# Kernel tuning notes

Measured on AMD Instinct MI355X. Metric: run time of the kernel, lower is better.

## Reference

```python
import jax, jax.numpy as jnp
import numpy as np

H, C = 2, 16          # heads, per-head channels (hidden_dim//2)
HD = H * C            # 32 = hidden_dim (concat heads)
NEG_SLOPE = 0.2       # PyG GATConv default negative_slope


def _gat(x, src, dst, edge_attr, lin_w, att_src, att_dst, edge_w, att_edge, bias):
    # Faithful PyG GATConv(in, C, heads=H, edge_dim=2, concat=True) in eval mode
    # (dropout inactive). add_self_loops=True with fill_value='mean' for edge_attr.
    N = x.shape[0]
    ones = jnp.ones((src.shape[0],), x.dtype)
    cnt = jax.ops.segment_sum(ones, dst, num_segments=N)
    mean_attr = jax.ops.segment_sum(edge_attr, dst, num_segments=N) / jnp.maximum(cnt, 1.0)[:, None]
    loop = jnp.arange(N, dtype=src.dtype)
    src_a = jnp.concatenate([src, loop])
    dst_a = jnp.concatenate([dst, loop])
    ea = jnp.concatenate([edge_attr, mean_attr], axis=0)            # [E+N, 2]
    xp = (x @ lin_w).reshape(N, H, C)                               # [N,H,C]
    a_src = (xp * att_src).sum(-1)                                  # [N,H]
    a_dst = (xp * att_dst).sum(-1)                                  # [N,H]
    ee = (ea @ edge_w).reshape(-1, H, C)                            # [E+N,H,C]
    a_edge = (ee * att_edge).sum(-1)                                # [E+N,H]
    alpha = jax.nn.leaky_relu(a_src[src_a] + a_dst[dst_a] + a_edge, NEG_SLOPE)
    m = jax.ops.segment_max(alpha, dst_a, num_segments=N)           # segment softmax over dst
    alpha = jnp.exp(alpha - m[dst_a])
    denom = jax.ops.segment_sum(alpha, dst_a, num_segments=N)
    alpha = alpha / (denom[dst_a] + 1e-16)
    msg = xp[src_a] * alpha[:, :, None]                             # [E+N,H,C]
    out = jax.ops.segment_sum(msg, dst_a, num_segments=N).reshape(N, HD)
    return out + bias


def _forward(group_ids, ord_feats, edge_index, edge_attr, pool_rows, pool_cols,
             pool_vals, P, embedding, g1, g2, g3, head_w1, head_b1, head_w2, head_b2):
    src, dst = edge_index[0], edge_index[1]
    x = jnp.concatenate([embedding[group_ids], ord_feats], axis=1)  # [N,20]
    h = jax.nn.relu(_gat(x, src, dst, edge_attr, *g1))
    h = jax.nn.relu(_gat(h, src, dst, edge_attr, *g2))
    h = jax.nn.relu(_gat(h, src, dst, edge_attr, *g3))              # [N,32]
    # sparse (P,N) Gaussian pooling matmul, COO form
    pooled = jax.ops.segment_sum(pool_vals[:, None] * h[pool_cols], pool_rows, num_segments=P)
    hh = jax.nn.relu(pooled @ head_w1 + head_b1)
    return (hh @ head_w2 + head_b2)[:, 0]                           # [P]


def setup_inputs() -> dict:
    key = jax.random.key(0)
    ks = jax.random.split(key, 32)
    N, E, P, NNZ, G = 100000, 3200000, 200000, 3200000, 19
    def nrm(k, shape, s=0.1):
        return jax.random.normal(k, shape, dtype=jnp.float32) * s
    inp = dict(
        group_ids=jax.random.randint(ks[0], (N,), 0, G, dtype=jnp.int32),
        ord_feats=jax.random.uniform(ks[1], (N, 4), dtype=jnp.float32),
        edge_index=jax.random.randint(ks[2], (2, E), 0, N, dtype=jnp.int32),
        edge_attr=jax.random.uniform(ks[3], (E, 2), dtype=jnp.float32),
        pool_rows=jax.random.randint(ks[4], (NNZ,), 0, P, dtype=jnp.int32),
        pool_cols=jax.random.randint(ks[5], (NNZ,), 0, N, dtype=jnp.int32),
        pool_vals=jax.random.uniform(ks[6], (NNZ,), dtype=jnp.float32),
        P=P,
        embedding=nrm(ks[7], (G, 16)),
    )
    ind = [20, HD, HD]
    for li in range(3):
        b = 8 + li * 6
        inp[f"g{li+1}_lin_w"] = nrm(ks[b], (ind[li], HD), (2.0 / (ind[li] + HD)) ** 0.5)
        inp[f"g{li+1}_att_src"] = nrm(ks[b + 1], (H, C))
        inp[f"g{li+1}_att_dst"] = nrm(ks[b + 2], (H, C))
        inp[f"g{li+1}_edge_w"] = nrm(ks[b + 3], (2, HD), 0.5)
        inp[f"g{li+1}_att_edge"] = nrm(ks[b + 4], (H, C))
        inp[f"g{li+1}_bias"] = jnp.zeros((HD,), jnp.float32)
    inp["head_w1"] = nrm(ks[26], (HD, 32), (2.0 / 64) ** 0.5)
    inp["head_b1"] = jnp.zeros((32,), jnp.float32)
    inp["head_w2"] = nrm(ks[27], (32, 1), (2.0 / 33) ** 0.5)
    inp["head_b2"] = jnp.zeros((1,), jnp.float32)
    return inp


def reference(group_ids, ord_feats, edge_index, edge_attr, pool_rows, pool_cols, pool_vals, P,
              embedding,
              g1_lin_w, g1_att_src, g1_att_dst, g1_edge_w, g1_att_edge, g1_bias,
              g2_lin_w, g2_att_src, g2_att_dst, g2_edge_w, g2_att_edge, g2_bias,
              g3_lin_w, g3_att_src, g3_att_dst, g3_edge_w, g3_att_edge, g3_bias,
              head_w1, head_b1, head_w2, head_b2):
    g1 = (g1_lin_w, g1_att_src, g1_att_dst, g1_edge_w, g1_att_edge, g1_bias)
    g2 = (g2_lin_w, g2_att_src, g2_att_dst, g2_edge_w, g2_att_edge, g2_bias)
    g3 = (g3_lin_w, g3_att_src, g3_att_dst, g3_edge_w, g3_att_edge, g3_bias)
    return _forward(group_ids, ord_feats, edge_index, edge_attr, pool_rows, pool_cols,
                    pool_vals, P, embedding, g1, g2, g3, head_w1, head_b1, head_w2, head_b2)
```

## Files before the change

### kernel.cpp

```cpp
#include <hip/hip_runtime.h>
#include <hip/hip_fp16.h>

#define TPB 256
#define STPB 1024
#define TILE 8192

__device__ __forceinline__ float leaky02(float x){ return x > 0.f ? x : 0.2f*x; }
__device__ __forceinline__ unsigned pack_h2(float a, float b){
  return (unsigned)__half_as_ushort(__float2half_rn(a)) |
         ((unsigned)__half_as_ushort(__float2half_rn(b)) << 16);
}

__global__ void k_scan_tile(const int* __restrict__ in, int* __restrict__ out,
                            int* __restrict__ bsum, int n) {
  __shared__ int sh[TPB];
  int t = threadIdx.x;
  int base = blockIdx.x * (TPB*4) + t*4;
  int v0=0,v1=0,v2=0,v3=0;
  if (base+0 < n) v0 = in[base+0];
  if (base+1 < n) v1 = in[base+1];
  if (base+2 < n) v2 = in[base+2];
  if (base+3 < n) v3 = in[base+3];
  int tsum = v0+v1+v2+v3;
  sh[t] = tsum; __syncthreads();
  for (int off=1; off<TPB; off<<=1){
    int x = (t>=off) ? sh[t-off] : 0;
    __syncthreads();
    sh[t] += x;
    __syncthreads();
  }
  int incl = sh[t];
  int excl = incl - tsum;
  if (t == TPB-1) bsum[blockIdx.x] = incl;
  int run = excl;
  if (base+0 < n){ out[base+0] = run; run += v0; }
  if (base+1 < n){ out[base+1] = run; run += v1; }
  if (base+2 < n){ out[base+2] = run; run += v2; }
  if (base+3 < n){ out[base+3] = run; run += v3; }
}

__global__ void k_scan_small(int* __restrict__ a, int n) {
  __shared__ int sh[TPB];
  __shared__ int carry;
  int t = threadIdx.x;
  if (t==0) carry = 0;
  __syncthreads();
  for (int base=0; base<n; base+=TPB){
    int v = (base+t < n) ? a[base+t] : 0;
    sh[t] = v; __syncthreads();
    for (int off=1; off<TPB; off<<=1){
      int x = (t>=off)? sh[t-off]:0; __syncthreads();
      sh[t]+=x; __syncthreads();
    }
    int c0 = carry;
    if (base+t < n) a[base+t] = c0 + sh[t] - v;
    int tot = sh[TPB-1];
    __syncthreads();
    if (t==0) carry = c0 + tot;
    __syncthreads();
  }
}

__global__ void k_scan_add(int* __restrict__ out, const int* __restrict__ bsum,
                           int n, int total) {
  int i = blockIdx.x*TPB + threadIdx.x;
  if (i < n) out[i] += bsum[i >> 10];
  if (i == 0) out[n] = total;
}

__global__ __launch_bounds__(STPB) void k_split_hist(
    const int* __restrict__ key, int n, int shift, int T,
    int* __restrict__ hist, int nbc){
  __shared__ int cnt[512];
  int b = blockIdx.x, t = threadIdx.x;
  for (int k=t;k<nbc;k+=STPB) cnt[k]=0;
  __syncthreads();
  int i0 = b*TILE, end = min(n, i0+TILE);
  for (int i=i0+t; i<end; i+=STPB) atomicAdd(&cnt[key[i]>>shift], 1);
  __syncthreads();
  for (int k=t;k<nbc;k+=STPB) hist[(size_t)k*T + b] = cnt[k];
}

__global__ __launch_bounds__(STPB) void k_split_scatter_edges(
    const int* __restrict__ src, const int* __restrict__ dst,
    const float* __restrict__ eattr, int E, int T,
    const int* __restrict__ hist, int2* __restrict__ tmp, int nbc){
  __shared__ int nxt[512];
  int b = blockIdx.x, t = threadIdx.x;
  for (int k=t;k<nbc;k+=STPB) nxt[k] = hist[(size_t)k*T + b];
  __syncthreads();
  int i0 = b*TILE, end = min(E, i0+TILE);
  for (int i=i0+t; i<end; i+=STPB){
    int d = dst[i];
    int k = d>>8;
    int pos = atomicAdd(&nxt[k], 1);
    float2 ea = ((const float2*)eattr)[i];
    tmp[pos] = make_int2(src[i] | ((d & 255)<<17), (int)pack_h2(ea.x, ea.y));
  }
}

__global__ __launch_bounds__(STPB) void k_split_scatter_pool(
    const int* __restrict__ rows, const int* __restrict__ cols,
    const float* __restrict__ vals, int n, int T,
    const int* __restrict__ hist, int2* __restrict__ tmp, int nbc){
  __shared__ int nxt[512];
  int b = blockIdx.x, t = threadIdx.x;
  for (int k=t;k<nbc;k+=STPB) nxt[k] = hist[(size_t)k*T + b];
  __syncthreads();
  int i0 = b*TILE, end = min(n, i0+TILE);
  for (int i=i0+t; i<end; i+=STPB){
    int r = rows[i];
    int k = r>>9;
    int pos = atomicAdd(&nxt[k], 1);
    tmp[pos] = make_int2(cols[i] | ((r & 511)<<17), __float_as_int(vals[i]));
  }
}

__global__ __launch_bounds__(STPB) void k_finalize_edges(
    const int2* __restrict__ tmp, const int* __restrict__ hist, int T, int E,
    int N, int* __restrict__ rs, int2* __restrict__ rec){
  __shared__ int cnt[256];
  __shared__ int sh[256];
  int b = blockIdx.x, t = threadIdx.x;
  int base = hist[(size_t)b*T];
  int endv = (b+1 < (int)gridDim.x) ? hist[(size_t)(b+1)*T] : E;
  int size = endv - base;
  if (t < 256) cnt[t] = 0;
  __syncthreads();
  for (int i=t; i<size; i+=STPB) atomicAdd(&cnt[(((unsigned)tmp[base+i].x)>>17)&255], 1);
  __syncthreads();
  int v = 0;
  if (t < 256){ v = cnt[t]; sh[t] = v; }
  __syncthreads();
  for (int off=1; off<256; off<<=1){
    int x = 0;
    if (t < 256 && t >= off) x = sh[t-off];
    __syncthreads();
    if (t < 256) sh[t] += x;
    __syncthreads();
  }
  if (t < 256){
    int excl = sh[t] - v;
    int d = (b<<8)+t;
    if (d<=N) rs[d] = base + excl;
    cnt[t] = excl;
  }
  __syncthreads();
  for (int i=t; i<size; i+=STPB){
    int2 q = tmp[base+i];
    int k = (((unsigned)q.x)>>17)&255;
    int p = atomicAdd(&cnt[k],1);
    rec[base+p] = make_int2(q.x & 0x1FFFF, q.y);
  }
}

__global__ __launch_bounds__(STPB) void k_finalize_pool(
    const int2* __restrict__ tmp, const int* __restrict__ hist, int T, int NNZ,
    int P, int* __restrict__ rs, int2* __restrict__ rec){
  __shared__ int cnt[512];
  __shared__ int sh[256];
  __shared__ int carry_s;
  int b = blockIdx.x, t = threadIdx.x;
  int base = hist[(size_t)b*T];
  int endv = (b+1 < (int)gridDim.x) ? hist[(size_t)(b+1)*T] : NNZ;
  int size = endv - base;
  if (t < 512) cnt[t] = 0;
  __syncthreads();
  for (int i=t;i<size;i+=STPB) atomicAdd(&cnt[(((unsigned)tmp[base+i].x)>>17)&511], 1);
  __syncthreads();
  int excl0 = 0, excl1 = 0;
  int v0 = 0;
  if (t < 256){ v0 = cnt[t]; sh[t] = v0; }
  __syncthreads();
  for (int off=1; off<256; off<<=1){
    int x = 0;
    if (t < 256 && t >= off) x = sh[t-off];
    __syncthreads();
    if (t < 256) sh[t] += x;
    __syncthreads();
  }
  if (t < 256) excl0 = sh[t] - v0;
  if (t == 255) carry_s = sh[255];
  __syncthreads();
  int v1 = 0;
  if (t < 256){ v1 = cnt[256+t]; sh[t] = v1; }
  __syncthreads();
  for (int off=1; off<256; off<<=1){
    int x = 0;
    if (t < 256 && t >= off) x = sh[t-off];
    __syncthreads();
    if (t < 256) sh[t] += x;
    __syncthreads();
  }
  if (t < 256) excl1 = carry_s + sh[t] - v1;
  __syncthreads();
  if (t < 256){
    cnt[t] = excl0; cnt[256+t] = excl1;
    int r0 = (b<<9)+t;
    if (r0<=P) rs[r0] = base+excl0;
    int r1 = r0+256;
    if (r1<=P) rs[r1] = base+excl1;
  }
  __syncthreads();
  for (int i=t;i<size;i+=STPB){
    int2 q = tmp[base+i];
    int k = (((unsigned)q.x)>>17)&511;
    int p = atomicAdd(&cnt[k],1);
    rec[base+p] = make_int2(q.x & 0x1FFFF, q.y);
  }
}

__global__ void k_weff(const float* __restrict__ ew1, const float* __restrict__ ae1,
                       const float* __restrict__ ew2, const float* __restrict__ ae2,
                       const float* __restrict__ ew3, const float* __restrict__ ae3,
                       float* __restrict__ weff){
  int t = threadIdx.x;
  if (t >= 6) return;
  int l = t>>1, h = t&1;
  const float* ew = l==0?ew1:(l==1?ew2:ew3);
  const float* ae = l==0?ae1:(l==1?ae2:ae3);
  float w0=0.f, w1=0.f;
  for (int c=0;c<16;c++){
    float a = ae[h*16+c];
    w0 += ew[h*16+c]*a;
    w1 += ew[32+h*16+c]*a;
  }
  weff[l*4+h*2]   = w0;
  weff[l*4+h*2+1] = w1;
}

__global__ __launch_bounds__(TPB) void k_node_pre1(
    const int* __restrict__ gid, const float* __restrict__ ord, const float* __restrict__ emb,
    const float* __restrict__ lin_w, const float* __restrict__ att_src, const float* __restrict__ att_dst,
    __half* __restrict__ xp16, float* __restrict__ asrc, float* __restrict__ adst, int N){
  __shared__ float W[20*32];
  __shared__ float As[32], Ad[32];
  for (int i=threadIdx.x; i<20*32; i+=TPB) W[i]=lin_w[i];
  if (threadIdx.x < 32){ As[threadIdx.x]=att_src[threadIdx.x]; Ad[threadIdx.x]=att_dst[threadIdx.x]; }
  __syncthreads();
  int n = blockIdx.x*TPB+threadIdx.x;
  if (n>=N) return;
  float x[20];
  int g = gid[n];
  #pragma unroll
  for (int k=0;k<16;k++) x[k]=emb[g*16+k];
  float4 o4 = ((const float4*)ord)[n];
  x[16]=o4.x; x[17]=o4.y; x[18]=o4.z; x[19]=o4.w;
  float acc[32];
  #pragma unroll
  for (int c=0;c<32;c++) acc[c]=0.f;
  #pragma unroll
  for (int k=0;k<20;k++){
    float xk=x[k];
    #pragma unroll
    for (int c=0;c<32;c++) acc[c] += xk*W[k*32+c];
  }
  float s0=0,s1=0,d0=0,d1=0;
  #pragma unroll
  for (int c=0;c<16;c++){
    s0+=acc[c]*As[c];      d0+=acc[c]*Ad[c];
    s1+=acc[16+c]*As[16+c]; d1+=acc[16+c]*Ad[16+c];
  }
  unsigned us[16];
  #pragma unroll
  for (int k=0;k<16;k++) us[k] = pack_h2(acc[2*k], acc[2*k+1]);
  uint4* o = (uint4*)(xp16 + (size_t)n*32);
  o[0]=make_uint4(us[0],us[1],us[2],us[3]);
  o[1]=make_uint4(us[4],us[5],us[6],us[7]);
  o[2]=make_uint4(us[8],us[9],us[10],us[11]);
  o[3]=make_uint4(us[12],us[13],us[14],us[15]);
  asrc[2*n]=s0; asrc[2*n+1]=s1; adst[2*n]=d0; adst[2*n+1]=d1;
}

__global__ __launch_bounds__(TPB) void k_node_pre(
    const float* __restrict__ hin,
    const float* __restrict__ lin_w, const float* __restrict__ att_src, const float* __restrict__ att_dst,
    __half* __restrict__ xp16, float* __restrict__ asrc, float* __restrict__ adst, int N){
  __shared__ float W[32*32];
  __shared__ float As[32], Ad[32];
  for (int i=threadIdx.x; i<1024; i+=TPB) W[i]=lin_w[i];
  if (threadIdx.x < 32){ As[threadIdx.x]=att_src[threadIdx.x]; Ad[threadIdx.x]=att_dst[threadIdx.x]; }
  __syncthreads();
  int n = blockIdx.x*TPB+threadIdx.x;
  if (n>=N) return;
  float x[32];
  const float4* hi = (const float4*)(hin + (size_t)n*32);
  #pragma unroll
  for (int q=0;q<8;q++){ float4 v=hi[q]; x[4*q]=v.x; x[4*q+1]=v.y; x[4*q+2]=v.z; x[4*q+3]=v.w; }
  float acc[32];
  #pragma unroll
  for (int c=0;c<32;c++) acc[c]=0.f;
  #pragma unroll
  for (int k=0;k<32;k++){
    float xk=x[k];
    #pragma unroll
    for (int c=0;c<32;c++) acc[c] += xk*W[k*32+c];
  }
  float s0=0,s1=0,d0=0,d1=0;
  #pragma unroll
  for (int c=0;c<16;c++){
    s0+=acc[c]*As[c];       d0+=acc[c]*Ad[c];
    s1+=acc[16+c]*As[16+c]; d1+=acc[16+c]*Ad[16+c];
  }
  unsigned us[16];
  #pragma unroll
  for (int k=0;k<16;k++) us[k] = pack_h2(acc[2*k], acc[2*k+1]);
  uint4* o = (uint4*)(xp16 + (size_t)n*32);
  o[0]=make_uint4(us[0],us[1],us[2],us[3]);
  o[1]=make_uint4(us[4],us[5],us[6],us[7]);
  o[2]=make_uint4(us[8],us[9],us[10],us[11]);
  o[3]=make_uint4(us[12],us[13],us[14],us[15]);
  asrc[2*n]=s0; asrc[2*n+1]=s1; adst[2*n]=d0; adst[2*n+1]=d1;
}

__global__ __launch_bounds__(TPB) void k_agg(
    const __half* __restrict__ xp16, const float* __restrict__ asrc, const float* __restrict__ adst,
    const int* __restrict__ rs, const int2* __restrict__ rec,
    const float* __restrict__ weff_l,
    const float* __restrict__ bias, float* __restrict__ houtf, __half* __restrict__ hout16, int N)
{
  int n = blockIdx.x*4 + (threadIdx.x>>6);
  if (n >= N) return;
  int lane = threadIdx.x & 63;
  int l4   = lane & 3;
  int quad = lane >> 2;
  int h    = l4 >> 1;
  float2 wv = ((const float2*)weff_l)[h];
  float adn = adst[2*n+h];
  float ax0=0,ay0=0,ax1=0,ay1=0,ax2=0,ay2=0,ax3=0,ay3=0;
  float den=0.f, sax=0.f, say=0.f;
  int jb = rs[n], je = rs[n+1];
  int j = jb + quad;
  for (; j + 16 < je; j += 32){
    int2 r1 = rec[j];
    int2 r2 = rec[j+16];
    uint4 u1 = ((const uint4*)(xp16 + (size_t)r1.x*32))[l4];
    uint4 u2 = ((const uint4*)(xp16 + (size_t)r2.x*32))[l4];
    float as1 = asrc[2*r1.x+h];
    float as2 = asrc[2*r2.x+h];
    float2 e1 = __half22float2(*(const __half2*)&r1.y);
    float2 e2 = __half22float2(*(const __half2*)&r2.y);
    sax += e1.x + e2.x; say += e1.y + e2.y;
    float p1 = __expf(leaky02(as1 + adn + e1.x*wv.x + e1.y*wv.y));
    float p2 = __expf(leaky02(as2 + adn + e2.x*wv.x + e2.y*wv.y));
    float2 f;
    f=__half22float2(*(const __half2*)&u1.x); ax0+=p1*f.x; ay0+=p1*f.y;
    f=__half22float2(*(const __half2*)&u1.y); ax1+=p1*f.x; ay1+=p1*f.y;
    f=__half22float2(*(const __half2*)&u1.z); ax2+=p1*f.x; ay2+=p1*f.y;
    f=__half22float2(*(const __half2*)&u1.w); ax3+=p1*f.x; ay3+=p1*f.y;
    f=__half22float2(*(const __half2*)&u2.x); ax0+=p2*f.x; ay0+=p2*f.y;
    f=__half22float2(*(const __half2*)&u2.y); ax1+=p2*f.x; ay1+=p2*f.y;
    f=__half22float2(*(const __half2*)&u2.z); ax2+=p2*f.x; ay2+=p2*f.y;
    f=__half22float2(*(const __half2*)&u2.w); ax3+=p2*f.x; ay3+=p2*f.y;
    den += p1 + p2;
  }
  if (j < je){
    int2 r1 = rec[j];
    uint4 u1 = ((const uint4*)(xp16 + (size_t)r1.x*32))[l4];
    float as1 = asrc[2*r1.x+h];
    float2 e1 = __half22float2(*(const __half2*)&r1.y);
    sax += e1.x; say += e1.y;
    float p1 = __expf(leaky02(as1 + adn + e1.x*wv.x + e1.y*wv.y));
    float2 f;
    f=__half22float2(*(const __half2*)&u1.x); ax0+=p1*f.x; ay0+=p1*f.y;
    f=__half22float2(*(const __half2*)&u1.y); ax1+=p1*f.x; ay1+=p1*f.y;
    f=__half22float2(*(const __half2*)&u1.z); ax2+=p1*f.x; ay2+=p1*f.y;
    f=__half22float2(*(const __half2*)&u1.w); ax3+=p1*f.x; ay3+=p1*f.y;
    den += p1;
  }
  #pragma unroll
  for (int m=4; m<64; m<<=1){
    ax0+=__shfl_xor(ax0,m); ay0+=__shfl_xor(ay0,m);
    ax1+=__shfl_xor(ax1,m); ay1+=__shfl_xor(ay1,m);
    ax2+=__shfl_xor(ax2,m); ay2+=__shfl_xor(ay2,m);
    ax3+=__shfl_xor(ax3,m); ay3+=__shfl_xor(ay3,m);
    den+=__shfl_xor(den,m);
    sax+=__shfl_xor(sax,m); say+=__shfl_xor(say,m);
  }
  if (quad == 0){
    int cn = je - jb;
    float inv = 1.0f / (float)(cn > 0 ? cn : 1);
    float al = leaky02(asrc[2*n+h] + adn + sax*inv*wv.x + say*inv*wv.y);
    float p = __expf(al);
    uint4 u = ((const uint4*)(xp16 + (size_t)n*32))[l4];
    float2 f0 = __half22float2(*(const __half2*)&u.x);
    float2 f1 = __half22float2(*(const __half2*)&u.y);
    float2 f2 = __half22float2(*(const __half2*)&u.z);
    float2 f3 = __half22float2(*(const __half2*)&u.w);
    ax0 += p*f0.x; ay0 += p*f0.y;
    ax1 += p*f1.x; ay1 += p*f1.y;
    ax2 += p*f2.x; ay2 += p*f2.y;
    ax3 += p*f3.x; ay3 += p*f3.y;
    den += p;
    float dinv = 1.0f/(den + 1e-16f);
    float4 b0 = ((const float4*)bias)[l4*2];
    float4 b1 = ((const float4*)bias)[l4*2+1];
    float o0 = fmaxf(ax0*dinv + b0.x, 0.f);
    float o1 = fmaxf(ay0*dinv + b0.y, 0.f);
    float o2 = fmaxf(ax1*dinv + b0.z, 0.f);
    float o3 = fmaxf(ay1*dinv + b0.w, 0.f);
    float o4 = fmaxf(ax2*dinv + b1.x, 0.f);
    float o5 = fmaxf(ay2*dinv + b1.y, 0.f);
    float o6 = fmaxf(ax3*dinv + b1.z, 0.f);
    float o7 = fmaxf(ay3*dinv + b1.w, 0.f);
    if (houtf){
      float4* o = (float4*)(houtf + (size_t)n*32);
      o[l4*2]   = make_float4(o0,o1,o2,o3);
      o[l4*2+1] = make_float4(o4,o5,o6,o7);
    }
    if (hout16){
      ((uint4*)(hout16 + (size_t)n*32))[l4] =
        make_uint4(pack_h2(o0,o1), pack_h2(o2,o3), pack_h2(o4,o5), pack_h2(o6,o7));
    }
  }
}

__global__ __launch_bounds__(TPB) void k_pool_q(
    const __half* __restrict__ h3, const int* __restrict__ rsP,
    const int2* __restrict__ rec, float* __restrict__ pooled, int P){
  int p = blockIdx.x*(TPB/4) + (threadIdx.x>>2);
  if (p >= P) return;
  int l4 = threadIdx.x & 3;
  float ax0=0,ay0=0,ax1=0,ay1=0,ax2=0,ay2=0,ax3=0,ay3=0;
  int jb = rsP[p], je = rsP[p+1];
  int j = jb;
  for (; j+1 < je; j += 2){
    int2 q1 = rec[j];
    int2 q2 = rec[j+1];
    uint4 u1 = ((const uint4*)(h3 + (size_t)q1.x*32))[l4];
    uint4 u2 = ((const uint4*)(h3 + (size_t)q2.x*32))[l4];
    float v1 = __int_as_float(q1.y);
    float v2 = __int_as_float(q2.y);
    float2 f;
    f=__half22float2(*(const __half2*)&u1.x); ax0+=v1*f.x; ay0+=v1*f.y;
    f=__half22float2(*(const __half2*)&u1.y); ax1+=v1*f.x; ay1+=v1*f.y;
    f=__half22float2(*(const __half2*)&u1.z); ax2+=v1*f.x; ay2+=v1*f.y;
    f=__half22float2(*(const __half2*)&u1.w); ax3+=v1*f.x; ay3+=v1*f.y;
    f=__half22float2(*(const __half2*)&u2.x); ax0+=v2*f.x; ay0+=v2*f.y;
    f=__half22float2(*(const __half2*)&u2.y); ax1+=v2*f.x; ay1+=v2*f.y;
    f=__half22float2(*(const __half2*)&u2.z); ax2+=v2*f.x; ay2+=v2*f.y;
    f=__half22float2(*(const __half2*)&u2.w); ax3+=v2*f.x; ay3+=v2*f.y;
  }
  if (j < je){
    int2 q1 = rec[j];
    uint4 u1 = ((const uint4*)(h3 + (size_t)q1.x*32))[l4];
    float v1 = __int_as_float(q1.y);
    float2 f;
    f=__half22float2(*(const __half2*)&u1.x); ax0+=v1*f.x; ay0+=v1*f.y;
    f=__half22float2(*(const __half2*)&u1.y); ax1+=v1*f.x; ay1+=v1*f.y;
    f=__half22float2(*(const __half2*)&u1.z); ax2+=v1*f.x; ay2+=v1*f.y;
    f=__half22float2(*(const __half2*)&u1.w); ax3+=v1*f.x; ay3+=v1*f.y;
  }
  float4* o = (float4*)(pooled + (size_t)p*32);
  o[l4*2]   = make_float4(ax0,ay0,ax1,ay1);
  o[l4*2+1] = make_float4(ax2,ay2,ax3,ay3);
}

__global__ __launch_bounds__(TPB) void k_head(
    const float* __restrict__ pooled,
    const float* __restrict__ W1, const float* __restrict__ b1,
    const float* __restrict__ W2, const float* __restrict__ b2,
    float* __restrict__ out, int P){
  __shared__ float sW1[32*32];
  __shared__ float sb1[32], sW2[32];
  for (int i=threadIdx.x;i<1024;i+=TPB) sW1[i]=W1[i];
  if (threadIdx.x<32){ sb1[threadIdx.x]=b1[threadIdx.x]; sW2[threadIdx.x]=W2[threadIdx.x]; }
  __syncthreads();
  int p = blockIdx.x*TPB + threadIdx.x;
  if (p >= P) return;
  float x[32];
  const float4* pi = (const float4*)(pooled + (size_t)p*32);
  #pragma unroll
  for (int q=0;q<8;q++){ float4 v=pi[q]; x[4*q]=v.x; x[4*q+1]=v.y; x[4*q+2]=v.z; x[4*q+3]=v.w; }
  float r = 0.f;
  #pragma unroll
  for (int c=0;c<32;c++){
    float hh = sb1[c];
    #pragma unroll
    for (int k=0;k<32;k++) hh += x[k]*sW1[k*32+c];
    r += fmaxf(hh, 0.f) * sW2[c];
  }
  out[p] = r + b2[0];
}

extern "C" void kernel_launch(void* const* d_in, const int* in_sizes, int n_in,
                              void* d_out, int out_size, void* d_ws, size_t ws_size,
                              hipStream_t stream){
  const int*   group_ids = (const int*)d_in[0];
  const float* ord       = (const float*)d_in[1];
  const int*   eidx      = (const int*)d_in[2];
  const float* eattr     = (const float*)d_in[3];
  const int*   prow      = (const int*)d_in[4];
  const int*   pcol      = (const int*)d_in[5];
  const float* pval      = (const float*)d_in[6];
  const float* emb       = (const float*)d_in[8];
  const float* head_w1   = (const float*)d_in[27];
  const float* head_b1   = (const float*)d_in[28];
  const float* head_w2   = (const float*)d_in[29];
  const float* head_b2   = (const float*)d_in[30];

  int N   = in_sizes[0];
  int E   = in_sizes[2]/2;
  int NNZ = in_sizes[4];
  int P   = out_size;

  const int* src = eidx;
  const int* dst = eidx + E;

  int NBC_E = (N+255)>>8;
  int T_E   = (E + TILE-1)/TILE;
  int nHistE = NBC_E*T_E;
  int NBC_P = (P+511)>>9;
  int T_P   = (NNZ + TILE-1)/TILE;
  int nHistP = NBC_P*T_P;
  int nHistMax = nHistE > nHistP ? nHistE : nHistP;
  size_t recMax = (size_t)(E > NNZ ? E : NNZ);

  char* w = (char*)d_ws;
  auto alloc = [&](size_t bytes)->char*{ char* p=w; w += (bytes+255)&~255ull; return p; };
  int*    hist = (int*)   alloc(4ull*(nHistMax+16));
  int*    bsum = (int*)   alloc(4ull*4096);
  int*    rs   = (int*)   alloc(4ull*(N+1));
  int*    rsP  = (int*)   alloc(4ull*(P+1));
  int2*   rec  = (int2*)  alloc(8ull*recMax);
  int2*   tmp  = (int2*)  alloc(8ull*recMax);
  __half* xp16 = (__half*)alloc(2ull*32*N);
  float*  asrc = (float*) alloc(8ull*N);
  float*  adst = (float*) alloc(8ull*N);
  float*  hbuf = (float*) alloc(4ull*32*N);
  float*  weff = (float*) alloc(256);
  __half* h316 = (__half*)hbuf;
  float*  pooled = (float*)tmp;

  int gN = (N+TPB-1)/TPB;

  k_split_hist<<<T_E,STPB,0,stream>>>(dst, E, 8, T_E, hist, NBC_E);
  int nbE = (nHistE+1023)/1024;
  k_scan_tile<<<nbE,TPB,0,stream>>>(hist, hist, bsum, nHistE);
  k_scan_small<<<1,TPB,0,stream>>>(bsum, nbE);
  k_scan_add<<<(nHistE+TPB-1)/TPB,TPB,0,stream>>>(hist, bsum, nHistE, E);
  k_split_scatter_edges<<<T_E,STPB,0,stream>>>(src, dst, eattr, E, T_E, hist, tmp, NBC_E);
  k_finalize_edges<<<NBC_E,STPB,0,stream>>>(tmp, hist, T_E, E, N, rs, rec);

  k_weff<<<1,64,0,stream>>>((const float*)d_in[12], (const float*)d_in[13],
                            (const float*)d_in[18], (const float*)d_in[19],
                            (const float*)d_in[24], (const float*)d_in[25], weff);

  k_node_pre1<<<gN,TPB,0,stream>>>(group_ids, ord, emb,
      (const float*)d_in[9], (const float*)d_in[10], (const float*)d_in[11],
      xp16, asrc, adst, N);
  int gagg = (N+3)/4;
  k_agg<<<gagg,TPB,0,stream>>>(xp16, asrc, adst, rs, rec, weff+0,
      (const float*)d_in[14], hbuf, (__half*)nullptr, N);
  k_node_pre<<<gN,TPB,0,stream>>>(hbuf,
      (const float*)d_in[15], (const float*)d_in[16], (const float*)d_in[17],
      xp16, asrc, adst, N);
  k_agg<<<gagg,TPB,0,stream>>>(xp16, asrc, adst, rs, rec, weff+4,
      (const float*)d_in[20], hbuf, (__half*)nullptr, N);
  k_node_pre<<<gN,TPB,0,stream>>>(hbuf,
      (const float*)d_in[21], (const float*)d_in[22], (const float*)d_in[23],
      xp16, asrc, adst, N);
  k_agg<<<gagg,TPB,0,stream>>>(xp16, asrc, adst, rs, rec, weff+8,
      (const float*)d_in[26], (float*)nullptr, h316, N);

  k_split_hist<<<T_P,STPB,0,stream>>>(prow, NNZ, 9, T_P, hist, NBC_P);
  int nbP = (nHistP+1023)/1024;
  k_scan_tile<<<nbP,TPB,0,stream>>>(hist, hist, bsum, nHistP);
  k_scan_small<<<1,TPB,0,stream>>>(bsum, nbP);
  k_scan_add<<<(nHistP+TPB-1)/TPB,TPB,0,stream>>>(hist, bsum, nHistP, NNZ);
  k_split_scatter_pool<<<T_P,STPB,0,stream>>>(prow, pcol, pval, NNZ, T_P, hist, tmp, NBC_P);
  k_finalize_pool<<<NBC_P,STPB,0,stream>>>(tmp, hist, T_P, NNZ, P, rsP, rec);

  int gpq = (P + TPB/4 - 1)/(TPB/4);
  k_pool_q<<<gpq,TPB,0,stream>>>(h316, rsP, rec, pooled, P);
  k_head<<<(P+TPB-1)/TPB,TPB,0,stream>>>(pooled,
      head_w1, head_b1, head_w2, head_b2, (float*)d_out, P);
}
```

Measured before the change: 436.5 us.

## Precompute mean self-loop edge attributes and pack four nodes per wavefront in aggregation

The per-destination mean of edge attributes is now accumulated once in the CSR finalize kernel through shared-memory atomics and stored in a per-node buffer, so the three aggregation passes no longer sum and reduce it. The aggregation kernel is remapped from one 64-lane wavefront per node to 16 lanes per node (four edge sub-lanes), with a shorter shuffle reduction. This is meant to cut wasted lanes on low-degree nodes and redundant work across layers. It costs some extra float atomics in finalize and lowers per-node parallelism for high-degree nodes.

After: 448.0 us. 1.03x slower.

```diff
diff --git a/kernel.cpp b/kernel.cpp
--- a/kernel.cpp
+++ b/kernel.cpp
@@ -118,16 +118,25 @@
 
 __global__ __launch_bounds__(STPB) void k_finalize_edges(
     const int2* __restrict__ tmp, const int* __restrict__ hist, int T, int E,
-    int N, int* __restrict__ rs, int2* __restrict__ rec){
+    int N, int* __restrict__ rs, int2* __restrict__ rec, float2* __restrict__ mattr){
   __shared__ int cnt[256];
   __shared__ int sh[256];
+  __shared__ float satt[512];
   int b = blockIdx.x, t = threadIdx.x;
   int base = hist[(size_t)b*T];
   int endv = (b+1 < (int)gridDim.x) ? hist[(size_t)(b+1)*T] : E;
   int size = endv - base;
   if (t < 256) cnt[t] = 0;
-  __syncthreads();
-  for (int i=t; i<size; i+=STPB) atomicAdd(&cnt[(((unsigned)tmp[base+i].x)>>17)&255], 1);
+  if (t < 512) satt[t] = 0.f;
+  __syncthreads();
+  for (int i=t; i<size; i+=STPB){
+    int2 q = tmp[base+i];
+    int ld = (((unsigned)q.x)>>17)&255;
+    atomicAdd(&cnt[ld], 1);
+    float2 ea = __half22float2(*(const __half2*)&q.y);
+    atomicAdd(&satt[2*ld],   ea.x);
+    atomicAdd(&satt[2*ld+1], ea.y);
+  }
   __syncthreads();
   int v = 0;
   if (t < 256){ v = cnt[t]; sh[t] = v; }
@@ -143,6 +152,10 @@
     int excl = sh[t] - v;
     int d = (b<<8)+t;
     if (d<=N) rs[d] = base + excl;
+    if (d<N){
+      float inv = 1.0f/(float)(v>0?v:1);
+      mattr[d] = make_float2(satt[2*t]*inv, satt[2*t+1]*inv);
+    }
     cnt[t] = excl;
   }
   __syncthreads();
@@ -316,31 +329,32 @@
 __global__ __launch_bounds__(TPB) void k_agg(
     const __half* __restrict__ xp16, const float* __restrict__ asrc, const float* __restrict__ adst,
     const int* __restrict__ rs, const int2* __restrict__ rec,
+    const float2* __restrict__ mattr,
     const float* __restrict__ weff_l,
     const float* __restrict__ bias, float* __restrict__ houtf, __half* __restrict__ hout16, int N)
 {
-  int n = blockIdx.x*4 + (threadIdx.x>>6);
+  int lane = threadIdx.x & 63;
+  int node_slot = lane >> 4;
+  int n = blockIdx.x*16 + (threadIdx.x>>6)*4 + node_slot;
   if (n >= N) return;
-  int lane = threadIdx.x & 63;
-  int l4   = lane & 3;
-  int quad = lane >> 2;
-  int h    = l4 >> 1;
+  int sub = (lane >> 2) & 3;
+  int l4  = lane & 3;
+  int h   = l4 >> 1;
   float2 wv = ((const float2*)weff_l)[h];
   float adn = adst[2*n+h];
   float ax0=0,ay0=0,ax1=0,ay1=0,ax2=0,ay2=0,ax3=0,ay3=0;
-  float den=0.f, sax=0.f, say=0.f;
+  float den=0.f;
   int jb = rs[n], je = rs[n+1];
-  int j = jb + quad;
-  for (; j + 16 < je; j += 32){
+  int j = jb + sub;
+  for (; j + 4 < je; j += 8){
     int2 r1 = rec[j];
-    int2 r2 = rec[j+16];
+    int2 r2 = rec[j+4];
     uint4 u1 = ((const uint4*)(xp16 + (size_t)r1.x*32))[l4];
     uint4 u2 = ((const uint4*)(xp16 + (size_t)r2.x*32))[l4];
     float as1 = asrc[2*r1.x+h];
     float as2 = asrc[2*r2.x+h];
     float2 e1 = __half22float2(*(const __half2*)&r1.y);
     float2 e2 = __half22float2(*(const __half2*)&r2.y);
-    sax += e1.x + e2.x; say += e1.y + e2.y;
     float p1 = __expf(leaky02(as1 + adn + e1.x*wv.x + e1.y*wv.y));
     float p2 = __expf(leaky02(as2 + adn + e2.x*wv.x + e2.y*wv.y));
     float2 f;
@@ -359,7 +373,6 @@
     uint4 u1 = ((const uint4*)(xp16 + (size_t)r1.x*32))[l4];
     float as1 = asrc[2*r1.x+h];
     float2 e1 = __half22float2(*(const __half2*)&r1.y);
-    sax += e1.x; say += e1.y;
     float p1 = __expf(leaky02(as1 + adn + e1.x*wv.x + e1.y*wv.y));
     float2 f;
     f=__half22float2(*(const __half2*)&u1.x); ax0+=p1*f.x; ay0+=p1*f.y;
@@ -369,18 +382,16 @@
     den += p1;
   }
   #pragma unroll
-  for (int m=4; m<64; m<<=1){
+  for (int m=4; m<16; m<<=1){
     ax0+=__shfl_xor(ax0,m); ay0+=__shfl_xor(ay0,m);
     ax1+=__shfl_xor(ax1,m); ay1+=__shfl_xor(ay1,m);
     ax2+=__shfl_xor(ax2,m); ay2+=__shfl_xor(ay2,m);
     ax3+=__shfl_xor(ax3,m); ay3+=__shfl_xor(ay3,m);
     den+=__shfl_xor(den,m);
-    sax+=__shfl_xor(sax,m); say+=__shfl_xor(say,m);
-  }
-  if (quad == 0){
-    int cn = je - jb;
-    float inv = 1.0f / (float)(cn > 0 ? cn : 1);
-    float al = leaky02(asrc[2*n+h] + adn + sax*inv*wv.x + say*inv*wv.y);
+  }
+  if (sub == 0){
+    float2 ma = mattr[n];
+    float al = leaky02(asrc[2*n+h] + adn + ma.x*wv.x + ma.y*wv.y);
     float p = __expf(al);
     uint4 u = ((const uint4*)(xp16 + (size_t)n*32))[l4];
     float2 f0 = __half22float2(*(const __half2*)&u.x);
@@ -529,6 +540,7 @@
   float*  adst = (float*) alloc(8ull*N);
   float*  hbuf = (float*) alloc(4ull*32*N);
   float*  weff = (float*) alloc(256);
+  float2* mattr= (float2*)alloc(8ull*N);
   __half* h316 = (__half*)hbuf;
   float*  pooled = (float*)tmp;
 
@@ -540,7 +552,7 @@
   k_scan_small<<<1,TPB,0,stream>>>(bsum, nbE);
   k_scan_add<<<(nHistE+TPB-1)/TPB,TPB,0,stream>>>(hist, bsum, nHistE, E);
   k_split_scatter_edges<<<T_E,STPB,0,stream>>>(src, dst, eattr, E, T_E, hist, tmp, NBC_E);
-  k_finalize_edges<<<NBC_E,STPB,0,stream>>>(tmp, hist, T_E, E, N, rs, rec);
+  k_finalize_edges<<<NBC_E,STPB,0,stream>>>(tmp, hist, T_E, E, N, rs, rec, mattr);
 
   k_weff<<<1,64,0,stream>>>((const float*)d_in[12], (const float*)d_in[13],
                             (const float*)d_in[18], (const float*)d_in[19],
@@ -549,18 +561,18 @@
   k_node_pre1<<<gN,TPB,0,stream>>>(group_ids, ord, emb,
       (const float*)d_in[9], (const float*)d_in[10], (const float*)d_in[11],
       xp16, asrc, adst, N);
-  int gagg = (N+3)/4;
-  k_agg<<<gagg,TPB,0,stream>>>(xp16, asrc, adst, rs, rec, weff+0,
+  int gagg = (N+15)/16;
+  k_agg<<<gagg,TPB,0,stream>>>(xp16, asrc, adst, rs, rec, mattr, weff+0,
       (const float*)d_in[14], hbuf, (__half*)nullptr, N);
   k_node_pre<<<gN,TPB,0,stream>>>(hbuf,
       (const float*)d_in[15], (const float*)d_in[16], (const float*)d_in[17],
       xp16, asrc, adst, N);
-  k_agg<<<gagg,TPB,0,stream>>>(xp16, asrc, adst, rs, rec, weff+4,
+  k_agg<<<gagg,TPB,0,stream>>>(xp16, asrc, adst, rs, rec, mattr, weff+4,
       (const float*)d_in[20], hbuf, (__half*)nullptr, N);
   k_node_pre<<<gN,TPB,0,stream>>>(hbuf,
       (const float*)d_in[21], (const float*)d_in[22], (const float*)d_in[23],
       xp16, asrc, adst, N);
-  k_agg<<<gagg,TPB,0,stream>>>(xp16, asrc, adst, rs, rec, weff+8,
+  k_agg<<<gagg,TPB,0,stream>>>(xp16, asrc, adst, rs, rec, mattr, weff+8,
       (const float*)d_in[26], (float*)nullptr, h316, N);
 
   k_split_hist<<<T_P,STPB,0,stream>>>(prow, NNZ, 9, T_P, hist, NBC_P);
```
